# Kernel optimization log

Measured on AMD Instinct MI355X. Metric: run time of the kernel, lower is better.

## Reference

```python
import jax, jax.numpy as jnp
import numpy as np

HIDDEN = 1280
HEADS = 16
HEAD_DIM = HIDDEN // HEADS  # 80
B, N = 2, 2048


def _rotate_half(x):
    half = x.shape[-1] // 2
    return jnp.concatenate([-x[..., half:], x[..., :half]], axis=-1)


def setup_inputs() -> dict:
    key = jax.random.key(0)
    ks = jax.random.split(key, 7)
    x = jax.random.normal(ks[0], (B, N, HIDDEN), dtype=jnp.float32)
    cos = jax.random.uniform(ks[1], (N, HEAD_DIM), dtype=jnp.float32)
    sin = jax.random.uniform(ks[2], (N, HEAD_DIM), dtype=jnp.float32)
    s = 1.0 / np.sqrt(HIDDEN)
    qkv_w = jax.random.normal(ks[3], (HIDDEN, 3 * HIDDEN), dtype=jnp.float32) * s
    qkv_b = jax.random.normal(ks[4], (3 * HIDDEN,), dtype=jnp.float32) * 0.02
    proj_w = jax.random.normal(ks[5], (HIDDEN, HIDDEN), dtype=jnp.float32) * s
    proj_b = jax.random.normal(ks[6], (HIDDEN,), dtype=jnp.float32) * 0.02
    return {"x": x, "cos": cos, "sin": sin, "qkv_w": qkv_w, "qkv_b": qkv_b,
            "proj_w": proj_w, "proj_b": proj_b}


def reference(x, cos, sin, qkv_w, qkv_b, proj_w, proj_b):
    b, n, _ = x.shape
    scale = 1.0 / np.sqrt(HEAD_DIM).astype(np.float32)
    # fused QKV projection
    qkv = x @ qkv_w + qkv_b                                # [b, n, 3*hidden]
    qkv = qkv.reshape(b, n, 3, HEADS, HEAD_DIM)
    qkv = jnp.transpose(qkv, (2, 0, 3, 1, 4))              # [3, b, h, n, hd]
    q, k, v = qkv[0], qkv[1], qkv[2]
    # 2D RoPE
    cos_b = cos[None, None, :, :]
    sin_b = sin[None, None, :, :]
    q = q * cos_b + _rotate_half(q) * sin_b
    k = k * cos_b + _rotate_half(k) * sin_b
    # manual softmax attention
    scores = jnp.einsum('bhqd,bhkd->bhqk', q, k) * scale   # [b, h, n, n]
    attn = jax.nn.softmax(scores, axis=-1)
    out = jnp.einsum('bhqk,bhkd->bhqd', attn, v)           # [b, h, n, hd]
    out = jnp.transpose(out, (0, 2, 1, 3)).reshape(b, n, HIDDEN)
    return out @ proj_w + proj_b
```

## Files before the change

kernel.cpp:

```cpp
#include <hip/hip_runtime.h>
#include <hip/hip_bf16.h>
#include <math.h>

#define HIDDEN 1280
#define HEADS 16
#define HD 80
#define HALF 40
#define BB 2
#define NN 2048
#define MROWS (BB * NN)
#define QSCALE ((float)(0.11180339887498949 * 1.4426950408889634))

typedef __attribute__((ext_vector_type(8))) _Float16 f16x8;
typedef __attribute__((ext_vector_type(4))) float f32x4;

#define AS1 __attribute__((address_space(1)))
#define AS3 __attribute__((address_space(3)))

__device__ __forceinline__ void splitf16(float x, ushort& hi, ushort& lo) {
    _Float16 h = (_Float16)x;
    _Float16 l = (_Float16)(x - (float)h);
    hi = __builtin_bit_cast(ushort, h);
    lo = __builtin_bit_cast(ushort, l);
}

__device__ __forceinline__ ushort f2h(float x) {
    _Float16 h = (_Float16)x;
    return __builtin_bit_cast(ushort, h);
}

__global__ __launch_bounds__(256) void split_f16_kernel(
    const float* __restrict__ in, ushort* __restrict__ hi,
    ushort* __restrict__ lo, int n4)
{
    int i = blockIdx.x * 256 + threadIdx.x;
    if (i >= n4) return;
    float4 v = ((const float4*)in)[i];
    ushort4 h, l;
    splitf16(v.x, h.x, l.x);
    splitf16(v.y, h.y, l.y);
    splitf16(v.z, h.z, l.z);
    splitf16(v.w, h.w, l.w);
    ((ushort4*)hi)[i] = h;
    ((ushort4*)lo)[i] = l;
}

__global__ __launch_bounds__(256) void tsplit_f16_kernel(
    const float* __restrict__ W, ushort* __restrict__ T, int K, int N)
{
    __shared__ float s[32][33];
    const int n0 = blockIdx.x * 32;
    const int k0 = blockIdx.y * 32;
    {
        int tn = threadIdx.x & 31, tk = threadIdx.x >> 5;
        #pragma unroll
        for (int i = 0; i < 4; ++i)
            s[tk + i * 8][tn] = W[(size_t)(k0 + tk + i * 8) * N + n0 + tn];
    }
    __syncthreads();
    {
        int tk = threadIdx.x & 31, tn = threadIdx.x >> 5;
        #pragma unroll
        for (int i = 0; i < 4; ++i)
            T[(size_t)(n0 + tn + i * 8) * K + k0 + tk] = f2h(s[tk][tn + i * 8]);
    }
}

#define BM 128
#define BN 128
#define BK 32

__global__ __launch_bounds__(256) void gemm_f16x2_kernel(
    const ushort* __restrict__ Ahi, const ushort* __restrict__ Alo,
    const ushort* __restrict__ Bh,
    const float* __restrict__ bias, float* __restrict__ C,
    int M, int N, int K)
{
    __shared__ __align__(16) ushort lds[3 * 128 * 32];

    const int tid = threadIdx.x;
    const int wid = tid >> 6;
    const int lane = tid & 63;
    const int col0 = blockIdx.x * BN;
    const int row0 = blockIdx.y * BM;
    const int wy = wid >> 1, wx = wid & 1;
    const int lrow = lane >> 2;
    const int lchunk = lane & 3;

    f32x4 acc[4][4] = {};

    for (int k0 = 0; k0 < K; k0 += BK) {
        __syncthreads();
        #pragma unroll
        for (int i = 0; i < 6; ++i) {
            int s = wid + i * 4;
            int tile = s >> 3, t = s & 7;
            const ushort* src = (tile == 0) ? Ahi : (tile == 1) ? Alo : Bh;
            int srow = (tile < 2) ? row0 : col0;
            const ushort* g = src + (size_t)(srow + t * 16 + lrow) * K + k0 + lchunk * 8;
            ushort* l = lds + tile * 4096 + t * 512 + lane * 8;
            __builtin_amdgcn_global_load_lds(
                (const AS1 unsigned int*)g, (AS3 unsigned int*)l, 16, 0, 0);
        }
        __syncthreads();

        const int q = lane >> 4;
        const int r = lane & 15;
        f16x8 ah[4], al[4], bf[4];
        #pragma unroll
        for (int i = 0; i < 4; ++i) {
            int arow = wy * 64 + i * 16 + r;
            ah[i] = *(const f16x8*)(lds + 0 * 4096 + arow * 32 + q * 8);
            al[i] = *(const f16x8*)(lds + 1 * 4096 + arow * 32 + q * 8);
            int brow = wx * 64 + i * 16 + r;
            bf[i] = *(const f16x8*)(lds + 2 * 4096 + brow * 32 + q * 8);
        }
        #pragma unroll
        for (int i = 0; i < 4; ++i) {
            #pragma unroll
            for (int j = 0; j < 4; ++j) {
                acc[i][j] = __builtin_amdgcn_mfma_f32_16x16x32_f16(al[i], bf[j], acc[i][j], 0, 0, 0);
                acc[i][j] = __builtin_amdgcn_mfma_f32_16x16x32_f16(ah[i], bf[j], acc[i][j], 0, 0, 0);
            }
        }
    }

    const int q = lane >> 4, r = lane & 15;
    #pragma unroll
    for (int i = 0; i < 4; ++i) {
        #pragma unroll
        for (int j = 0; j < 4; ++j) {
            int col = col0 + wx * 64 + j * 16 + r;
            float b = bias[col];
            #pragma unroll
            for (int v = 0; v < 4; ++v) {
                int row = row0 + wy * 64 + i * 16 + q * 4 + v;
                C[(size_t)row * N + col] = acc[i][j][v] + b;
            }
        }
    }
}

__global__ __launch_bounds__(512, 4) void gemm_f16x2_256x128_kernel(
    const ushort* __restrict__ Ahi, const ushort* __restrict__ Alo,
    const ushort* __restrict__ Bh,
    const float* __restrict__ bias, float* __restrict__ C,
    int M, int N, int K, int nbx)
{
    __shared__ __align__(16) ushort lds[2 * 20480];

    const int tid = threadIdx.x;
    const int wid = tid >> 6;
    const int lane = tid & 63;
    const int q = lane >> 4, r = lane & 15;
    const int wr = wid >> 1;
    const int wc = wid & 1;

    int id = blockIdx.x;
    {
        int nwg = gridDim.x;
        if ((nwg & 7) == 0) {
            int c = nwg >> 3;
            id = (id & 7) * c + (id >> 3);
        }
    }
    const int row0 = (id / nbx) * 256;
    const int col0 = (id % nbx) * 128;

    const ushort* gsrc[5];
    int ldst[5];
    #pragma unroll
    for (int j = 0; j < 5; ++j) {
        if (j < 4) {
            int p = j >> 1;
            int rloc = wid * 32 + (j & 1) * 16 + (lane >> 2);
            int sl = (lane & 3) ^ ((rloc >> 1) & 3);
            const ushort* base = p ? Alo : Ahi;
            gsrc[j] = base + (size_t)(row0 + rloc) * K + sl * 8;
            ldst[j] = p * 8192 + (wid * 32 + (j & 1) * 16) * 32 + lane * 8;
        } else {
            int rloc = wid * 16 + (lane >> 2);
            int sl = (lane & 3) ^ ((rloc >> 1) & 3);
            gsrc[4] = Bh + (size_t)(col0 + rloc) * K + sl * 8;
            ldst[4] = 16384 + wid * 512 + lane * 8;
        }
    }

    const int NT = K / 32;

    #pragma unroll
    for (int j = 0; j < 5; ++j)
        __builtin_amdgcn_global_load_lds((const AS1 unsigned int*)(gsrc[j]),
            (AS3 unsigned int*)(lds + ldst[j]), 16, 0, 0);
    asm volatile("s_waitcnt vmcnt(0)" ::: "memory");
    __builtin_amdgcn_s_barrier();

    const int soff = (q ^ ((r >> 1) & 3)) * 8;
    const int arow0 = wr * 64 + r;
    const int brow0 = wc * 64 + r;

    f32x4 acc[4][4] = {};
    f16x8 ah[4], al[4], bf[2];

    int cb = 0;
    for (int t = 0; t < NT; ++t) {
        const ushort* A0 = lds + cb;
        const ushort* A1 = lds + cb + 8192;
        const ushort* Bp = lds + cb + 16384;
        ushort* nbuf = lds + (20480 - cb);
        const bool st = (t + 1 < NT);
        const int ko = (t + 1) * 32;

        #pragma unroll
        for (int m = 0; m < 4; ++m) {
            int ro = (arow0 + m * 16) * 32 + soff;
            ah[m] = *(const f16x8*)(A0 + ro);
            al[m] = *(const f16x8*)(A1 + ro);
        }
        #pragma unroll
        for (int n = 0; n < 2; ++n)
            bf[n] = *(const f16x8*)(Bp + (brow0 + n * 16) * 32 + soff);
        if (st) {
            __builtin_amdgcn_global_load_lds((const AS1 unsigned int*)(gsrc[0] + ko),
                (AS3 unsigned int*)(nbuf + ldst[0]), 16, 0, 0);
            __builtin_amdgcn_global_load_lds((const AS1 unsigned int*)(gsrc[1] + ko),
                (AS3 unsigned int*)(nbuf + ldst[1]), 16, 0, 0);
            __builtin_amdgcn_global_load_lds((const AS1 unsigned int*)(gsrc[2] + ko),
                (AS3 unsigned int*)(nbuf + ldst[2]), 16, 0, 0);
        }
        __builtin_amdgcn_s_barrier();
        asm volatile("s_waitcnt lgkmcnt(0)" ::: "memory");
        __builtin_amdgcn_sched_barrier(0);
        __builtin_amdgcn_s_setprio(1);
        #pragma unroll
        for (int m = 0; m < 4; ++m) {
            #pragma unroll
            for (int n = 0; n < 2; ++n) {
                acc[m][n] = __builtin_amdgcn_mfma_f32_16x16x32_f16(al[m], bf[n], acc[m][n], 0, 0, 0);
                acc[m][n] = __builtin_amdgcn_mfma_f32_16x16x32_f16(ah[m], bf[n], acc[m][n], 0, 0, 0);
            }
        }
        __builtin_amdgcn_s_setprio(0);
        __builtin_amdgcn_s_barrier();

        #pragma unroll
        for (int n = 0; n < 2; ++n)
            bf[n] = *(const f16x8*)(Bp + (brow0 + (n + 2) * 16) * 32 + soff);
        if (st) {
            __builtin_amdgcn_global_load_lds((const AS1 unsigned int*)(gsrc[3] + ko),
                (AS3 unsigned int*)(nbuf + ldst[3]), 16, 0, 0);
            __builtin_amdgcn_global_load_lds((const AS1 unsigned int*)(gsrc[4] + ko),
                (AS3 unsigned int*)(nbuf + ldst[4]), 16, 0, 0);
        }
        __builtin_amdgcn_s_barrier();
        asm volatile("s_waitcnt lgkmcnt(0)" ::: "memory");
        __builtin_amdgcn_sched_barrier(0);
        __builtin_amdgcn_s_setprio(1);
        #pragma unroll
        for (int m = 0; m < 4; ++m) {
            #pragma unroll
            for (int n = 0; n < 2; ++n) {
                acc[m][n + 2] = __builtin_amdgcn_mfma_f32_16x16x32_f16(al[m], bf[n], acc[m][n + 2], 0, 0, 0);
                acc[m][n + 2] = __builtin_amdgcn_mfma_f32_16x16x32_f16(ah[m], bf[n], acc[m][n + 2], 0, 0, 0);
            }
        }
        __builtin_amdgcn_s_setprio(0);
        asm volatile("s_waitcnt vmcnt(0)" ::: "memory");
        __builtin_amdgcn_s_barrier();
        cb = 20480 - cb;
    }

    #pragma unroll
    for (int m = 0; m < 4; ++m) {
        #pragma unroll
        for (int n = 0; n < 4; ++n) {
            int col = col0 + wc * 64 + n * 16 + r;
            float b = bias[col];
            #pragma unroll
            for (int v = 0; v < 4; ++v) {
                int row = row0 + wr * 64 + m * 16 + q * 4 + v;
                C[(size_t)row * N + col] = acc[m][n][v] + b;
            }
        }
    }
}

__global__ __launch_bounds__(256) void rope_split_kernel(
    const float* __restrict__ qkv, const float* __restrict__ cos_t,
    const float* __restrict__ sin_t,
    ushort* __restrict__ qf, ushort* __restrict__ kf,
    ushort* __restrict__ vt)
{
    __shared__ float s_v[64][84];
    const int tid = threadIdx.x;
    const int b = blockIdx.z, h = blockIdx.y;
    const int n0 = blockIdx.x * 64;
    const int bh = b * HEADS + h;

    #pragma unroll
    for (int i = 0; i < 5; ++i) {
        int u = tid + i * 256;
        int n = u / 20, c = u % 20;
        const float* src = qkv + (size_t)(b * NN + n0 + n) * 3840 + 2 * HIDDEN + h * HD + c * 4;
        *(float4*)(&s_v[n][c * 4]) = *(const float4*)src;
    }

    for (int u = tid; u < 640; u += 256) {
        int n = u / 10, p = u % 10;
        int d = p * 4;
        int ng = n0 + n;
        size_t rowb = (size_t)(b * NN + ng) * 3840;
        float4 c0 = *(const float4*)(cos_t + ng * HD + d);
        float4 c1 = *(const float4*)(cos_t + ng * HD + d + HALF);
        float4 s0 = *(const float4*)(sin_t + ng * HD + d);
        float4 s1 = *(const float4*)(sin_t + ng * HD + d + HALF);
        size_t qo = ((size_t)bh * NN + ng) * 96;
        {
            float4 x0 = *(const float4*)(qkv + rowb + h * HD + d);
            float4 x1 = *(const float4*)(qkv + rowb + h * HD + d + HALF);
            ushort4 h4a, h4b;
            h4a.x = f2h((x0.x * c0.x - x1.x * s0.x) * QSCALE);
            h4a.y = f2h((x0.y * c0.y - x1.y * s0.y) * QSCALE);
            h4a.z = f2h((x0.z * c0.z - x1.z * s0.z) * QSCALE);
            h4a.w = f2h((x0.w * c0.w - x1.w * s0.w) * QSCALE);
            h4b.x = f2h((x1.x * c1.x + x0.x * s1.x) * QSCALE);
            h4b.y = f2h((x1.y * c1.y + x0.y * s1.y) * QSCALE);
            h4b.z = f2h((x1.z * c1.z + x0.z * s1.z) * QSCALE);
            h4b.w = f2h((x1.w * c1.w + x0.w * s1.w) * QSCALE);
            *(ushort4*)(qf + qo + d) = h4a;
            *(ushort4*)(qf + qo + d + HALF) = h4b;
        }
        {
            float4 x0 = *(const float4*)(qkv + rowb + HIDDEN + h * HD + d);
            float4 x1 = *(const float4*)(qkv + rowb + HIDDEN + h * HD + d + HALF);
            ushort4 h4a, h4b;
            h4a.x = f2h(x0.x * c0.x - x1.x * s0.x);
            h4a.y = f2h(x0.y * c0.y - x1.y * s0.y);
            h4a.z = f2h(x0.z * c0.z - x1.z * s0.z);
            h4a.w = f2h(x0.w * c0.w - x1.w * s0.w);
            h4b.x = f2h(x1.x * c1.x + x0.x * s1.x);
            h4b.y = f2h(x1.y * c1.y + x0.y * s1.y);
            h4b.z = f2h(x1.z * c1.z + x0.z * s1.z);
            h4b.w = f2h(x1.w * c1.w + x0.w * s1.w);
            *(ushort4*)(kf + qo + d) = h4a;
            *(ushort4*)(kf + qo + d + HALF) = h4b;
        }
    }

    {
        int which = tid >> 7;
        int u = tid & 127;
        int n = u >> 1, part = u & 1;
        size_t o = ((size_t)bh * NN + n0 + n) * 96 + 80 + part * 8;
        uint4 z = {0u, 0u, 0u, 0u};
        if (which == 0) *(uint4*)(qf + o) = z;
        else            *(uint4*)(kf + o) = z;
    }
    __syncthreads();

    for (int u = tid; u < 320; u += 256) {
        int d = u >> 2, nc = u & 3;
        ushort hs[16];
        #pragma unroll
        for (int kk = 0; kk < 16; ++kk)
            hs[kk] = f2h(s_v[nc * 16 + kk][d]);
        size_t o = ((size_t)bh * HD + d) * NN + n0 + nc * 16;
        uint4 w0, w1;
        w0.x = (uint)hs[0] | ((uint)hs[1] << 16);
        w0.y = (uint)hs[2] | ((uint)hs[3] << 16);
        w0.z = (uint)hs[4] | ((uint)hs[5] << 16);
        w0.w = (uint)hs[6] | ((uint)hs[7] << 16);
        w1.x = (uint)hs[8] | ((uint)hs[9] << 16);
        w1.y = (uint)hs[10] | ((uint)hs[11] << 16);
        w1.z = (uint)hs[12] | ((uint)hs[13] << 16);
        w1.w = (uint)hs[14] | ((uint)hs[15] << 16);
        *(uint4*)(vt + o) = w0;
        *(uint4*)(vt + o + 8) = w1;
    }
}

__global__ __launch_bounds__(512, 4) void attn_mfma_kernel(
    const ushort* __restrict__ qf, const ushort* __restrict__ kf,
    const ushort* __restrict__ vt,
    ushort* __restrict__ ao_hi, ushort* __restrict__ ao_lo)
{
    __shared__ __align__(16) ushort lds[34816];
    _Float16* p_s = (_Float16*)(lds + 26624);

    const int tid = threadIdx.x;
    const int wave = tid >> 6, lane = tid & 63;
    const int quad = lane >> 4, r = lane & 15;
    const int b = blockIdx.z, h = blockIdx.y;
    const int bh = b * HEADS + h;
    const int q0 = blockIdx.x * 128;

    const size_t kb = (size_t)bh * NN * 96;
    const size_t vb = (size_t)bh * HD * NN;

    const ushort* gptr[4];
    int ldso[4];
    #pragma unroll
    for (int i = 0; i < 4; ++i) {
        int s = wave + i * 8;
        if (s < 16) {
            int row = s * 4 + (lane >> 4);
            int t = lane & 15;
            int g = t ^ (row & 7);
            if (g >= 12) g = 0;
            gptr[i] = kf + kb + (size_t)row * 96 + g * 8;
            ldso[i] = s * 512 + lane * 8;
        } else if (s < 26) {
            int ts = s - 16;
            gptr[i] = vt + vb + (size_t)(ts * 8 + (lane >> 3)) * NN
                      + (size_t)(((lane & 7) ^ (lane >> 3)) * 8);
            ldso[i] = 8192 + ts * 512 + lane * 8;
        } else {
            gptr[i] = nullptr;
            ldso[i] = 0;
        }
    }

    f16x8 qfr[3];
    #pragma unroll
    for (int c = 0; c < 3; ++c) {
        size_t o = ((size_t)bh * NN + q0 + wave * 16 + r) * 96 + c * 32 + quad * 8;
        qfr[c] = *(const f16x8*)(qf + o);
    }

    f32x4 oacc[5] = {};
    float l_part[4] = {};

    #pragma unroll
    for (int i = 0; i < 4; ++i) {
        int s = wave + i * 8;
        if (s < 26) {
            __builtin_amdgcn_global_load_lds((const AS1 unsigned int*)gptr[i],
                (AS3 unsigned int*)(lds + ldso[i]), 16, 0, 0);
            gptr[i] += (s < 16) ? 6144 : 64;
        }
    }
    asm volatile("s_waitcnt vmcnt(0)" ::: "memory");
    __builtin_amdgcn_s_barrier();

    int cur = 0;
    for (int j0 = 0; j0 < NN; j0 += 64) {
        const int nxt = 13312 - cur;
        if (j0 + 64 < NN) {
            #pragma unroll
            for (int i = 0; i < 4; ++i) {
                int s = wave + i * 8;
                if (s < 26) {
                    __builtin_amdgcn_global_load_lds((const AS1 unsigned int*)gptr[i],
                        (AS3 unsigned int*)(lds + nxt + ldso[i]), 16, 0, 0);
                    gptr[i] += (s < 16) ? 6144 : 64;
                }
            }
        }

        const ushort* k_s = lds + cur;
        const _Float16* v_s = (const _Float16*)(lds + cur + 8192);

        f32x4 sc[4] = {};
        __builtin_amdgcn_s_setprio(1);
        #pragma unroll
        for (int jt = 0; jt < 4; ++jt) {
            f16x8 kbf[3];
            int j = jt * 16 + r;
            #pragma unroll
            for (int c = 0; c < 3; ++c) {
                int ch = (c * 4 + quad) ^ (r & 7);
                kbf[c] = *(const f16x8*)(k_s + j * 128 + ch * 8);
            }
            #pragma unroll
            for (int c = 0; c < 3; ++c)
                sc[jt] = __builtin_amdgcn_mfma_f32_16x16x32_f16(qfr[c], kbf[c], sc[jt], 0, 0, 0);
        }
        __builtin_amdgcn_s_setprio(0);

        #pragma unroll
        for (int v = 0; v < 4; ++v) {
            float ps = 0.0f;
            #pragma unroll
            for (int jt = 0; jt < 4; ++jt) {
                float p = __builtin_amdgcn_exp2f(sc[jt][v]);
                sc[jt][v] = p;
                ps += p;
            }
            l_part[v] += ps;
        }
        {
            int rowbase = wave * 16 + quad * 4;
            #pragma unroll
            for (int jt = 0; jt < 4; ++jt) {
                int bks = (jt * 2 + (r >> 3)) ^ (quad << 1);
                #pragma unroll
                for (int v = 0; v < 4; ++v)
                    p_s[(rowbase + v) * 64 + bks * 8 + (r & 7)] = (_Float16)sc[jt][v];
            }
        }

        f16x8 pa[2];
        #pragma unroll
        for (int cc = 0; cc < 2; ++cc) {
            int rowp = wave * 16 + r;
            int bks = (cc * 4 + quad) ^ (((r >> 2) & 3) << 1);
            pa[cc] = *(const f16x8*)(p_s + rowp * 64 + bks * 8);
        }

        __builtin_amdgcn_s_setprio(1);
        #pragma unroll
        for (int dt = 0; dt < 5; ++dt)
            #pragma unroll
            for (int cc = 0; cc < 2; ++cc) {
                int ck = (cc * 4 + quad) ^ (r & 7);
                f16x8 vbf = *(const f16x8*)(v_s + (dt * 16 + r) * 64 + ck * 8);
                oacc[dt] = __builtin_amdgcn_mfma_f32_16x16x32_f16(pa[cc], vbf, oacc[dt], 0, 0, 0);
            }
        __builtin_amdgcn_s_setprio(0);

        asm volatile("s_waitcnt vmcnt(0)" ::: "memory");
        __builtin_amdgcn_s_barrier();
        cur = nxt;
    }

    float inv_l[4];
    #pragma unroll
    for (int v = 0; v < 4; ++v) {
        float l = l_part[v];
        l += __shfl_xor(l, 1);
        l += __shfl_xor(l, 2);
        l += __shfl_xor(l, 4);
        l += __shfl_xor(l, 8);
        inv_l[v] = 1.0f / l;
    }

    __syncthreads();
    #pragma unroll
    for (int v = 0; v < 4; ++v) {
        int row = wave * 16 + quad * 4 + v;
        #pragma unroll
        for (int dt = 0; dt < 5; ++dt) {
            float o = oacc[dt][v] * inv_l[v];
            ushort hh, ll;
            splitf16(o, hh, ll);
            lds[row * 80 + dt * 16 + r] = hh;
            lds[10240 + row * 80 + dt * 16 + r] = ll;
        }
    }
    __syncthreads();
    {
        size_t gbase = ((size_t)b * NN + q0) * HIDDEN + h * HD;
        #pragma unroll
        for (int i = 0; i < 5; ++i) {
            int u = tid + i * 512;
            int plane = u / 1280, idx = u % 1280;
            int row = idx / 10, part = idx % 10;
            uint4 w = *(const uint4*)(lds + plane * 10240 + idx * 8);
            ushort* dst = (plane ? ao_lo : ao_hi) + gbase + (size_t)row * HIDDEN + part * 8;
            *(uint4*)dst = w;
        }
    }
}

extern "C" void kernel_launch(void* const* d_in, const int* in_sizes, int n_in,
                              void* d_out, int out_size, void* d_ws, size_t ws_size,
                              hipStream_t stream)
{
    const float* x      = (const float*)d_in[0];
    const float* cos_t  = (const float*)d_in[1];
    const float* sin_t  = (const float*)d_in[2];
    const float* qkv_w  = (const float*)d_in[3];
    const float* qkv_b  = (const float*)d_in[4];
    const float* proj_w = (const float*)d_in[5];
    const float* proj_b = (const float*)d_in[6];
    float* out = (float*)d_out;

    char* ws = (char*)d_ws;
    float*  qkv   = (float*)ws;
    ushort* ao_hi = (ushort*)ws;
    ushort* ao_lo = (ushort*)(ws + 10485760);
    ushort* wT    = (ushort*)(ws + 62914560);
    ushort* vt    = (ushort*)(ws + 62914560);
    ushort* a_hi  = (ushort*)(ws + 82575360);
    ushort* a_lo  = (ushort*)(ws + 93061120);
    ushort* q_f   = (ushort*)(ws + 83886080);
    ushort* k_f   = (ushort*)(ws + 96468992);

    split_f16_kernel<<<(MROWS * HIDDEN / 4 + 255) / 256, 256, 0, stream>>>(
        x, a_hi, a_lo, MROWS * HIDDEN / 4);

    tsplit_f16_kernel<<<dim3(3 * HIDDEN / 32, HIDDEN / 32), 256, 0, stream>>>(
        qkv_w, wT, HIDDEN, 3 * HIDDEN);

    gemm_f16x2_256x128_kernel<<<dim3((MROWS / 256) * (3 * HIDDEN / 128)), 512, 0, stream>>>(
        a_hi, a_lo, wT, qkv_b, qkv, MROWS, 3 * HIDDEN, HIDDEN, 3 * HIDDEN / 128);

    rope_split_kernel<<<dim3(NN / 64, HEADS, BB), 256, 0, stream>>>(
        qkv, cos_t, sin_t, q_f, k_f, vt);

    attn_mfma_kernel<<<dim3(NN / 128, HEADS, BB), 512, 0, stream>>>(
        q_f, k_f, vt, ao_hi, ao_lo);

    tsplit_f16_kernel<<<dim3(HIDDEN / 32, HIDDEN / 32), 256, 0, stream>>>(
        proj_w, wT, HIDDEN, HIDDEN);

    gemm_f16x2_kernel<<<dim3(HIDDEN / BN, MROWS / BM), 256, 0, stream>>>(
        ao_hi, ao_lo, wT, proj_b, out, MROWS, HIDDEN, HIDDEN);
}
```

Before: 326.1 us.

## Load K/V fragments directly from global memory and remap blocks for L2 locality

The attention kernel no longer stages K and V tiles through double-buffered LDS with global_load_lds and per-tile barriers. Each wave now reads its K and V MFMA operands straight from global memory and relies on L2/cache reuse across the 8 waves. The launch grid is flattened and block ids are remapped so that consecutive blocks of the same head are spread across XCDs. This removes the barriers and lowers LDS use, which may raise occupancy, but each wave now issues redundant global loads and no longer prefetches the next tile.

```diff
diff --git a/kernel.cpp b/kernel.cpp
--- a/kernel.cpp
+++ b/kernel.cpp
@@ -384,41 +384,21 @@
     const ushort* __restrict__ vt,
     ushort* __restrict__ ao_hi, ushort* __restrict__ ao_lo)
 {
-    __shared__ __align__(16) ushort lds[34816];
-    _Float16* p_s = (_Float16*)(lds + 26624);
+    __shared__ __align__(16) ushort lds[20480];
+    _Float16* p_s = (_Float16*)lds;
 
     const int tid = threadIdx.x;
     const int wave = tid >> 6, lane = tid & 63;
     const int quad = lane >> 4, r = lane & 15;
-    const int b = blockIdx.z, h = blockIdx.y;
-    const int bh = b * HEADS + h;
-    const int q0 = blockIdx.x * 128;
+
+    int id = blockIdx.x;
+    id = (id & 7) * 64 + (id >> 3);
+    const int bh = id >> 4;
+    const int q0 = (id & 15) * 128;
+    const int b = bh >> 4, h = bh & 15;
 
     const size_t kb = (size_t)bh * NN * 96;
     const size_t vb = (size_t)bh * HD * NN;
-
-    const ushort* gptr[4];
-    int ldso[4];
-    #pragma unroll
-    for (int i = 0; i < 4; ++i) {
-        int s = wave + i * 8;
-        if (s < 16) {
-            int row = s * 4 + (lane >> 4);
-            int t = lane & 15;
-            int g = t ^ (row & 7);
-            if (g >= 12) g = 0;
-            gptr[i] = kf + kb + (size_t)row * 96 + g * 8;
-            ldso[i] = s * 512 + lane * 8;
-        } else if (s < 26) {
-            int ts = s - 16;
-            gptr[i] = vt + vb + (size_t)(ts * 8 + (lane >> 3)) * NN
-                      + (size_t)(((lane & 7) ^ (lane >> 3)) * 8);
-            ldso[i] = 8192 + ts * 512 + lane * 8;
-        } else {
-            gptr[i] = nullptr;
-            ldso[i] = 0;
-        }
-    }
 
     f16x8 qfr[3];
     #pragma unroll
@@ -430,47 +410,19 @@
     f32x4 oacc[5] = {};
     float l_part[4] = {};
 
-    #pragma unroll
-    for (int i = 0; i < 4; ++i) {
-        int s = wave + i * 8;
-        if (s < 26) {
-            __builtin_amdgcn_global_load_lds((const AS1 unsigned int*)gptr[i],
-                (AS3 unsigned int*)(lds + ldso[i]), 16, 0, 0);
-            gptr[i] += (s < 16) ? 6144 : 64;
-        }
-    }
-    asm volatile("s_waitcnt vmcnt(0)" ::: "memory");
-    __builtin_amdgcn_s_barrier();
-
-    int cur = 0;
+    const ushort* kp = kf + kb + (size_t)r * 96 + quad * 8;
+    const ushort* vp = vt + vb + (size_t)(r)*NN;
+
     for (int j0 = 0; j0 < NN; j0 += 64) {
-        const int nxt = 13312 - cur;
-        if (j0 + 64 < NN) {
-            #pragma unroll
-            for (int i = 0; i < 4; ++i) {
-                int s = wave + i * 8;
-                if (s < 26) {
-                    __builtin_amdgcn_global_load_lds((const AS1 unsigned int*)gptr[i],
-                        (AS3 unsigned int*)(lds + nxt + ldso[i]), 16, 0, 0);
-                    gptr[i] += (s < 16) ? 6144 : 64;
-                }
-            }
-        }
-
-        const ushort* k_s = lds + cur;
-        const _Float16* v_s = (const _Float16*)(lds + cur + 8192);
-
         f32x4 sc[4] = {};
         __builtin_amdgcn_s_setprio(1);
         #pragma unroll
         for (int jt = 0; jt < 4; ++jt) {
             f16x8 kbf[3];
-            int j = jt * 16 + r;
-            #pragma unroll
-            for (int c = 0; c < 3; ++c) {
-                int ch = (c * 4 + quad) ^ (r & 7);
-                kbf[c] = *(const f16x8*)(k_s + j * 128 + ch * 8);
-            }
+            const ushort* kr = kp + (size_t)(j0 + jt * 16) * 96;
+            #pragma unroll
+            for (int c = 0; c < 3; ++c)
+                kbf[c] = *(const f16x8*)(kr + c * 32);
             #pragma unroll
             for (int c = 0; c < 3; ++c)
                 sc[jt] = __builtin_amdgcn_mfma_f32_16x16x32_f16(qfr[c], kbf[c], sc[jt], 0, 0, 0);
@@ -509,18 +461,15 @@
 
         __builtin_amdgcn_s_setprio(1);
         #pragma unroll
-        for (int dt = 0; dt < 5; ++dt)
+        for (int dt = 0; dt < 5; ++dt) {
+            const ushort* vr = vp + (size_t)(dt * 16) * NN + j0;
             #pragma unroll
             for (int cc = 0; cc < 2; ++cc) {
-                int ck = (cc * 4 + quad) ^ (r & 7);
-                f16x8 vbf = *(const f16x8*)(v_s + (dt * 16 + r) * 64 + ck * 8);
+                f16x8 vbf = *(const f16x8*)(vr + (cc * 4 + quad) * 8);
                 oacc[dt] = __builtin_amdgcn_mfma_f32_16x16x32_f16(pa[cc], vbf, oacc[dt], 0, 0, 0);
             }
+        }
         __builtin_amdgcn_s_setprio(0);
-
-        asm volatile("s_waitcnt vmcnt(0)" ::: "memory");
-        __builtin_amdgcn_s_barrier();
-        cur = nxt;
     }
 
     float inv_l[4];
@@ -598,7 +547,7 @@
     rope_split_kernel<<<dim3(NN / 64, HEADS, BB), 256, 0, stream>>>(
         qkv, cos_t, sin_t, q_f, k_f, vt);
 
-    attn_mfma_kernel<<<dim3(NN / 128, HEADS, BB), 512, 0, stream>>>(
+    attn_mfma_kernel<<<dim3(512), 512, 0, stream>>>(
         q_f, k_f, vt, ao_hi, ao_lo);
 
     tsplit_f16_kernel<<<dim3(HIDDEN / 32, HIDDEN / 32), 256, 0, stream>>>(
```

Result: slower. 483.4 us (+48.2%).

## Triple-buffer QKV GEMM with register double-buffered fragments and one barrier per k-step

Applied to the files above, without the earlier changes.

Rewrites the QKV projection GEMM main loop from a two-buffer scheme with split half-tiles into a three-stage LDS ring. Fragments for the next k-step are read into a second register set while MFMAs run on the current set, and each k-step has a single sync point instead of several. The goal is to hide global-to-LDS latency and LDS reads behind the MFMA work. In exchange it uses more LDS (three buffers) and more registers, and launch bounds drop to 2 blocks per CU, which lowers occupancy.

```diff
diff --git a/kernel.cpp b/kernel.cpp
--- a/kernel.cpp
+++ b/kernel.cpp
@@ -141,13 +141,13 @@
     }
 }
 
-__global__ __launch_bounds__(512, 4) void gemm_f16x2_256x128_kernel(
+__global__ __launch_bounds__(512, 2) void gemm_f16x2_pipe_kernel(
     const ushort* __restrict__ Ahi, const ushort* __restrict__ Alo,
     const ushort* __restrict__ Bh,
     const float* __restrict__ bias, float* __restrict__ C,
     int M, int N, int K, int nbx)
 {
-    __shared__ __align__(16) ushort lds[2 * 20480];
+    __shared__ __align__(16) ushort lds[3 * 20480];
 
     const int tid = threadIdx.x;
     const int wid = tid >> 6;
@@ -186,88 +186,71 @@
         }
     }
 
-    const int NT = K / 32;
-
-    #pragma unroll
-    for (int j = 0; j < 5; ++j)
-        __builtin_amdgcn_global_load_lds((const AS1 unsigned int*)(gsrc[j]),
-            (AS3 unsigned int*)(lds + ldst[j]), 16, 0, 0);
-    asm volatile("s_waitcnt vmcnt(0)" ::: "memory");
-    __builtin_amdgcn_s_barrier();
-
     const int soff = (q ^ ((r >> 1) & 3)) * 8;
     const int arow0 = wr * 64 + r;
     const int brow0 = wc * 64 + r;
 
     f32x4 acc[4][4] = {};
-    f16x8 ah[4], al[4], bf[2];
-
-    int cb = 0;
-    for (int t = 0; t < NT; ++t) {
-        const ushort* A0 = lds + cb;
-        const ushort* A1 = lds + cb + 8192;
-        const ushort* Bp = lds + cb + 16384;
-        ushort* nbuf = lds + (20480 - cb);
-        const bool st = (t + 1 < NT);
-        const int ko = (t + 1) * 32;
-
+    f16x8 ahA[4], alA[4], bfA[4];
+    f16x8 ahB[4], alB[4], bfB[4];
+
+    auto stage = [&](int t, int bufbase) {
+        int ko = t * 32;
+        #pragma unroll
+        for (int j = 0; j < 5; ++j)
+            __builtin_amdgcn_global_load_lds((const AS1 unsigned int*)(gsrc[j] + ko),
+                (AS3 unsigned int*)(lds + bufbase + ldst[j]), 16, 0, 0);
+    };
+    auto read_frags = [&](f16x8* ah, f16x8* al, f16x8* bf, const ushort* base) {
         #pragma unroll
         for (int m = 0; m < 4; ++m) {
             int ro = (arow0 + m * 16) * 32 + soff;
-            ah[m] = *(const f16x8*)(A0 + ro);
-            al[m] = *(const f16x8*)(A1 + ro);
-        }
-        #pragma unroll
-        for (int n = 0; n < 2; ++n)
-            bf[n] = *(const f16x8*)(Bp + (brow0 + n * 16) * 32 + soff);
-        if (st) {
-            __builtin_amdgcn_global_load_lds((const AS1 unsigned int*)(gsrc[0] + ko),
-                (AS3 unsigned int*)(nbuf + ldst[0]), 16, 0, 0);
-            __builtin_amdgcn_global_load_lds((const AS1 unsigned int*)(gsrc[1] + ko),
-                (AS3 unsigned int*)(nbuf + ldst[1]), 16, 0, 0);
-            __builtin_amdgcn_global_load_lds((const AS1 unsigned int*)(gsrc[2] + ko),
-                (AS3 unsigned int*)(nbuf + ldst[2]), 16, 0, 0);
-        }
-        __builtin_amdgcn_s_barrier();
-        asm volatile("s_waitcnt lgkmcnt(0)" ::: "memory");
-        __builtin_amdgcn_sched_barrier(0);
+            ah[m] = *(const f16x8*)(base + ro);
+            al[m] = *(const f16x8*)(base + 8192 + ro);
+        }
+        #pragma unroll
+        for (int n = 0; n < 4; ++n)
+            bf[n] = *(const f16x8*)(base + 16384 + (brow0 + n * 16) * 32 + soff);
+    };
+    auto do_mfma = [&](f16x8* ah, f16x8* al, f16x8* bf) {
         __builtin_amdgcn_s_setprio(1);
         #pragma unroll
         for (int m = 0; m < 4; ++m) {
             #pragma unroll
-            for (int n = 0; n < 2; ++n) {
+            for (int n = 0; n < 4; ++n) {
                 acc[m][n] = __builtin_amdgcn_mfma_f32_16x16x32_f16(al[m], bf[n], acc[m][n], 0, 0, 0);
                 acc[m][n] = __builtin_amdgcn_mfma_f32_16x16x32_f16(ah[m], bf[n], acc[m][n], 0, 0, 0);
             }
         }
         __builtin_amdgcn_s_setprio(0);
-        __builtin_amdgcn_s_barrier();
-
-        #pragma unroll
-        for (int n = 0; n < 2; ++n)
-            bf[n] = *(const f16x8*)(Bp + (brow0 + (n + 2) * 16) * 32 + soff);
-        if (st) {
-            __builtin_amdgcn_global_load_lds((const AS1 unsigned int*)(gsrc[3] + ko),
-                (AS3 unsigned int*)(nbuf + ldst[3]), 16, 0, 0);
-            __builtin_amdgcn_global_load_lds((const AS1 unsigned int*)(gsrc[4] + ko),
-                (AS3 unsigned int*)(nbuf + ldst[4]), 16, 0, 0);
-        }
-        __builtin_amdgcn_s_barrier();
-        asm volatile("s_waitcnt lgkmcnt(0)" ::: "memory");
-        __builtin_amdgcn_sched_barrier(0);
-        __builtin_amdgcn_s_setprio(1);
-        #pragma unroll
-        for (int m = 0; m < 4; ++m) {
-            #pragma unroll
-            for (int n = 0; n < 2; ++n) {
-                acc[m][n + 2] = __builtin_amdgcn_mfma_f32_16x16x32_f16(al[m], bf[n], acc[m][n + 2], 0, 0, 0);
-                acc[m][n + 2] = __builtin_amdgcn_mfma_f32_16x16x32_f16(ah[m], bf[n], acc[m][n + 2], 0, 0, 0);
-            }
-        }
-        __builtin_amdgcn_s_setprio(0);
+    };
+
+    const int NT = K / 32;
+
+    stage(0, 0);
+    stage(1, 20480);
+    asm volatile("s_waitcnt vmcnt(5)" ::: "memory");
+    __builtin_amdgcn_s_barrier();
+    __builtin_amdgcn_sched_barrier(0);
+    read_frags(ahA, alA, bfA, lds);
+
+    int cb = 0, rb = 20480, sb = 40960;
+    for (int t = 0; t < NT; t += 2) {
         asm volatile("s_waitcnt vmcnt(0)" ::: "memory");
         __builtin_amdgcn_s_barrier();
-        cb = 20480 - cb;
+        __builtin_amdgcn_sched_barrier(0);
+        if (t + 2 < NT) stage(t + 2, sb);
+        read_frags(ahB, alB, bfB, lds + rb);
+        do_mfma(ahA, alA, bfA);
+        { int tmp = cb; cb = rb; rb = sb; sb = tmp; }
+
+        asm volatile("s_waitcnt vmcnt(0)" ::: "memory");
+        __builtin_amdgcn_s_barrier();
+        __builtin_amdgcn_sched_barrier(0);
+        if (t + 3 < NT) stage(t + 3, sb);
+        if (t + 2 < NT) read_frags(ahA, alA, bfA, lds + rb);
+        do_mfma(ahB, alB, bfB);
+        { int tmp = cb; cb = rb; rb = sb; sb = tmp; }
     }
 
     #pragma unroll
@@ -592,7 +575,7 @@
     tsplit_f16_kernel<<<dim3(3 * HIDDEN / 32, HIDDEN / 32), 256, 0, stream>>>(
         qkv_w, wT, HIDDEN, 3 * HIDDEN);
 
-    gemm_f16x2_256x128_kernel<<<dim3((MROWS / 256) * (3 * HIDDEN / 128)), 512, 0, stream>>>(
+    gemm_f16x2_pipe_kernel<<<dim3((MROWS / 256) * (3 * HIDDEN / 128)), 512, 0, stream>>>(
         a_hi, a_lo, wT, qkv_b, qkv, MROWS, 3 * HIDDEN, HIDDEN, 3 * HIDDEN / 128);
 
     rope_split_kernel<<<dim3(NN / 64, HEADS, BB), 256, 0, stream>>>(
```

After: 334.0 us. 2.4% more time.
